# Performance work log

Measured on AMD Instinct MI355X. Metric: run time of the kernel, lower is better.

## Reference

```python
import jax, jax.numpy as jnp
import numpy as np

CH = 512
GROUPS = 8
EPS = 1e-5


def setup_inputs() -> dict:
    key = jax.random.key(0)
    ks = jax.random.split(key, 5)
    B, C, H, W = 16, CH, 32, 32
    x = jax.random.normal(ks[0], (B, C, H, W), dtype=jnp.float32)
    # GroupNorm affine params
    norm_w = jnp.ones((C,), dtype=jnp.float32)
    norm_b = jnp.zeros((C,), dtype=jnp.float32)
    # 1x1 conv == linear over channels; store weights as [out, in]
    qkv_w = jax.random.normal(ks[1], (3 * C, C), dtype=jnp.float32) * (C ** -0.5)
    qkv_b = jnp.zeros((3 * C,), dtype=jnp.float32)
    proj_w = jax.random.normal(ks[2], (C, C), dtype=jnp.float32) * (C ** -0.5)
    proj_b = jnp.zeros((C,), dtype=jnp.float32)
    return {"x": x, "norm_w": norm_w, "norm_b": norm_b,
            "qkv_w": qkv_w, "qkv_b": qkv_b,
            "proj_w": proj_w, "proj_b": proj_b}


def _group_norm(x, w, b):
    B, C, H, W = x.shape
    g = GROUPS
    xg = x.reshape(B, g, C // g, H * W)
    mean = xg.mean(axis=(2, 3), keepdims=True)
    var = xg.var(axis=(2, 3), keepdims=True)
    xn = (xg - mean) * jax.lax.rsqrt(var + EPS)
    xn = xn.reshape(B, C, H, W)
    return xn * w[None, :, None, None] + b[None, :, None, None]


def reference(x, norm_w, norm_b, qkv_w, qkv_b, proj_w, proj_b):
    B, C, H, W = x.shape
    h = _group_norm(x, norm_w, norm_b)  # [B,C,H,W]
    hs = h.reshape(B, C, H * W)  # spatial tokens along last axis
    # 1x1 conv QKV: [3C,C] @ [B,C,N] -> [B,3C,N]
    qkv = jnp.einsum('oc,bcn->bon', qkv_w, hs) + qkv_b[None, :, None]
    q, k, v = jnp.split(qkv, 3, axis=1)  # each [B,C,N]
    scale = C ** (-0.5)
    attn = jnp.einsum('bci,bcj->bij', q, k) * scale  # [B,N,N]
    attn = jax.nn.softmax(attn, axis=-1)
    out = jnp.einsum('bij,bcj->bci', attn, v)  # [B,C,N]
    out = jnp.einsum('oc,bcn->bon', proj_w, out) + proj_b[None, :, None]
    return x + out.reshape(B, C, H, W)
```

## Files before the change

kernel.cpp:

```cpp
#include <hip/hip_runtime.h>
#include <math.h>

#define Bn   16
#define Cn   512
#define Nn   1024
#define Gn   8
#define CPG  64
#define EPSf 1e-5f

typedef short           bf16x8 __attribute__((ext_vector_type(8)));
typedef float           f32x4  __attribute__((ext_vector_type(4)));
typedef unsigned short  u16;
typedef unsigned short  u16x4  __attribute__((ext_vector_type(4)));
typedef unsigned short  u16x8  __attribute__((ext_vector_type(8)));

#define TS 136

__device__ __forceinline__ u16 f2b(float f) {
  union { float f; unsigned u; } c; c.f = f;
  unsigned r = (c.u + 0x7FFFu + ((c.u >> 16) & 1u)) >> 16;
  return (u16)r;
}

__device__ __forceinline__ void g2l16(const void* g, void* l) {
  __builtin_amdgcn_global_load_lds(
      (const __attribute__((address_space(1))) unsigned int*)g,
      (__attribute__((address_space(3))) unsigned int*)l, 16, 0, 0);
}

__device__ __forceinline__ void gemm_core(u16* As, u16* Bs,
    const u16* __restrict__ A, size_t sA,
    const u16* __restrict__ B, size_t sB, int K, f32x4 acc[4][4]) {
  const int t = threadIdx.x;
  const int w = t >> 6, l = t & 63, quad = l >> 4, lr = l & 15;
  const int wm = (w >> 1) * 64, wn = (w & 1) * 64;

  const int ra = w * 16 + (l >> 2);
  const int p  = l & 3;
  const int q  = p ^ ((ra >> 1) & 3);
  const u16* gA0 = A + (size_t)ra * sA + q * 8;
  const u16* gA1 = A + (size_t)(ra + 64) * sA + q * 8;
  const u16* gB0 = B + (size_t)ra * sB + q * 8;
  const u16* gB1 = B + (size_t)(ra + 64) * sB + q * 8;
  u16* lA0 = As + ra * 32 + p * 8;
  u16* lA1 = As + (ra + 64) * 32 + p * 8;
  u16* lB0 = Bs + ra * 32 + p * 8;
  u16* lB1 = Bs + (ra + 64) * 32 + p * 8;

  for (int k0 = 0; k0 < K; k0 += 32) {
    __syncthreads();
    g2l16(gA0 + k0, lA0);
    g2l16(gA1 + k0, lA1);
    g2l16(gB0 + k0, lB0);
    g2l16(gB1 + k0, lB1);
    __syncthreads();
    bf16x8 af[4], bfr[4];
    #pragma unroll
    for (int fm = 0; fm < 4; fm++) {
      int r = wm + fm * 16 + lr;
      af[fm] = *(const bf16x8*)&As[r * 32 + ((quad ^ ((r >> 1) & 3)) << 3)];
    }
    #pragma unroll
    for (int fn = 0; fn < 4; fn++) {
      int r = wn + fn * 16 + lr;
      bfr[fn] = *(const bf16x8*)&Bs[r * 32 + ((quad ^ ((r >> 1) & 3)) << 3)];
    }
    #pragma unroll
    for (int fm = 0; fm < 4; fm++)
      #pragma unroll
      for (int fn = 0; fn < 4; fn++)
        acc[fm][fn] = __builtin_amdgcn_mfma_f32_16x16x32_bf16(
            af[fm], bfr[fn], acc[fm][fn], 0, 0, 0);
  }
}

#define GEMM_PRE()                                              \
  const int t = threadIdx.x;                                    \
  const int w = t >> 6, l = t & 63, quad = l >> 4, lr = l & 15; \
  const int wm = (w >> 1) * 64, wn = (w & 1) * 64;              \
  (void)w; (void)wm; (void)wn; (void)l;                         \
  f32x4 acc[4][4];                                              \
  { f32x4 z = {0.f, 0.f, 0.f, 0.f};                             \
    for (int i_ = 0; i_ < 4; i_++)                              \
      for (int j_ = 0; j_ < 4; j_++) acc[i_][j_] = z; }

#define TILE_FLUSH(T, DST, rowstride)                           \
  {                                                             \
    _Pragma("unroll")                                           \
    for (int k_ = 0; k_ < 4; k_++) {                            \
      int idx = threadIdx.x + 256 * k_;                         \
      int row = idx >> 4, ch = idx & 15;                        \
      u16x8 v_ = *(u16x8*)&T[row * TS + ch * 8];                \
      *(u16x8*)&(DST)[(size_t)row * (rowstride) + ch * 8] = v_; \
    }                                                           \
  }

__global__ __launch_bounds__(256) void prep_k(const float* __restrict__ qkv_w,
    const float* __restrict__ proj_w, const float* __restrict__ qkv_b,
    const float* __restrict__ x, u16* __restrict__ wqk16,
    u16* __restrict__ wvT16, u16* __restrict__ pw16,
    float* __restrict__ bias2, float* __restrict__ stats) {
  __shared__ u16 T[64][68];
  __shared__ float redf[8];
  int bid = blockIdx.x, t = threadIdx.x;
  if (bid < 512) {
    int i = bid * 256 + t;
    float4 v = ((const float4*)qkv_w)[i];
    u16x4 o;
    o.x = f2b(v.x); o.y = f2b(v.y); o.z = f2b(v.z); o.w = f2b(v.w);
    ((u16x4*)wqk16)[i] = o;
  } else if (bid < 576) {
    int tile = bid - 512, tx = tile & 7, ty = tile >> 3;
    int row = t >> 4, col4 = t & 15;
    #pragma unroll
    for (int it = 0; it < 4; it++) {
      int cc = row + it * 16;
      float4 v = *(const float4*)&qkv_w[(size_t)(1024 + ty * 64 + cc) * 512 + tx * 64 + col4 * 4];
      u16x4 o;
      o.x = f2b(v.x); o.y = f2b(v.y); o.z = f2b(v.z); o.w = f2b(v.w);
      *(u16x4*)&T[cc][col4 * 4] = o;
    }
    __syncthreads();
    #pragma unroll
    for (int it = 0; it < 2; it++) {
      int ch = t + it * 256;
      int d = ch >> 3, c8 = (ch & 7) * 8;
      u16x8 o;
      #pragma unroll
      for (int j = 0; j < 8; j++) o[j] = T[c8 + j][d];
      *(u16x8*)&wvT16[(size_t)(tx * 64 + d) * 512 + ty * 64 + c8] = o;
    }
  } else if (bid < 578) {
    int m = (bid - 576) * 256 + t;
    float s = 0.f;
    for (int c = 0; c < 512; c++)
      s += proj_w[(size_t)m * 512 + c] * qkv_b[1024 + c];
    bias2[m] = s;
  } else if (bid < 1090) {
    int idx = bid - 578, bg = idx >> 2, part = idx & 3;
    const float4* xp = (const float4*)x + (size_t)bg * 16384 + part * 4096;
    float s = 0.f, ss = 0.f;
    for (int i = t; i < 4096; i += 256) {
      float4 v = xp[i];
      s  += v.x + v.y + v.z + v.w;
      ss += v.x * v.x + v.y * v.y + v.z * v.z + v.w * v.w;
    }
    #pragma unroll
    for (int off = 32; off > 0; off >>= 1) {
      s  += __shfl_down(s, off);
      ss += __shfl_down(ss, off);
    }
    int lane = t & 63, wid = t >> 6;
    if (lane == 0) { redf[wid] = s; redf[4 + wid] = ss; }
    __syncthreads();
    if (t == 0) {
      atomicAdd(&stats[bg],       redf[0] + redf[1] + redf[2] + redf[3]);
      atomicAdd(&stats[128 + bg], redf[4] + redf[5] + redf[6] + redf[7]);
    }
  } else {
    int i = (bid - 1090) * 256 + t;
    float4 v = ((const float4*)proj_w)[i];
    u16x4 o;
    o.x = f2b(v.x); o.y = f2b(v.y); o.z = f2b(v.z); o.w = f2b(v.w);
    ((u16x4*)pw16)[i] = o;
  }
}

__global__ __launch_bounds__(256) void gnw2_k(const float* __restrict__ x,
    const float* __restrict__ stats, const float* __restrict__ nw,
    const float* __restrict__ nb, const u16* __restrict__ pw16,
    const u16* __restrict__ wvT16, u16* __restrict__ W2, u16* __restrict__ hT) {
  __shared__ u16 AsBs[8192];
  int bid = blockIdx.x;
  if (bid < 16) {
    int m0 = (bid >> 2) * 128, d0 = (bid & 3) * 128;
    GEMM_PRE();
    gemm_core(AsBs, AsBs + 4096, pw16 + (size_t)m0 * 512, 512,
              wvT16 + (size_t)d0 * 512, 512, 512, acc);
    #pragma unroll
    for (int fm = 0; fm < 4; fm++) {
      int m = m0 + wm + fm * 16 + quad * 4;
      #pragma unroll
      for (int fn = 0; fn < 4; fn++) {
        int d = d0 + wn + fn * 16 + lr;
        f32x4 a = acc[fm][fn];
        W2[(size_t)(m    ) * 512 + d] = f2b(a[0]);
        W2[(size_t)(m + 1) * 512 + d] = f2b(a[1]);
        W2[(size_t)(m + 2) * 512 + d] = f2b(a[2]);
        W2[(size_t)(m + 3) * 512 + d] = f2b(a[3]);
      }
    }
    return;
  }
  int u = bid - 16;
  int b = u >> 7, rem = u & 127, c0 = (rem >> 4) * 64, n0 = (rem & 15) * 64;
  u16 (*T)[68] = (u16(*)[68])AsBs;
  int t = threadIdx.x;
  int row = t >> 4, col4 = t & 15;
  const float inv = 1.0f / 65536.0f;
  #pragma unroll
  for (int it = 0; it < 4; it++) {
    int cc = row + it * 16;
    int c  = c0 + cc;
    int bg = b * Gn + (c >> 6);
    float mean = stats[bg] * inv;
    float var  = stats[128 + bg] * inv - mean * mean;
    float rstd = rsqrtf(var + EPSf);
    float a  = nw[c] * rstd;
    float bb = nb[c] - mean * a;
    float4 xv = *(const float4*)&x[((size_t)(b * Cn + c)) * Nn + n0 + col4 * 4];
    u16x4 o;
    o.x = f2b(xv.x * a + bb); o.y = f2b(xv.y * a + bb);
    o.z = f2b(xv.z * a + bb); o.w = f2b(xv.w * a + bb);
    *(u16x4*)&T[cc][col4 * 4] = o;
  }
  __syncthreads();
  #pragma unroll
  for (int it = 0; it < 2; it++) {
    int ch = t + it * 256;
    int n  = ch >> 3, c8 = (ch & 7) * 8;
    u16x8 o;
    #pragma unroll
    for (int j = 0; j < 8; j++) o[j] = T[c8 + j][n];
    *(u16x8*)&hT[((size_t)(b * Nn + n0 + n)) * 512 + c0 + c8] = o;
  }
}

__global__ __launch_bounds__(256) void qkvp_k(const u16* __restrict__ wqk16,
    const u16* __restrict__ W2, const u16* __restrict__ hT,
    const float* __restrict__ qkv_b, u16* __restrict__ qkT,
    u16* __restrict__ VP) {
  __shared__ u16 SH[64 * TS];
  int u = blockIdx.x;
  GEMM_PRE();
  if (u < 1024) {
    int b = u >> 6, rem = u & 63, m0 = (rem >> 3) * 128, n0 = (rem & 7) * 128;
    gemm_core(SH, SH + 4096, wqk16 + (size_t)m0 * 512, 512,
              hT + ((size_t)(b * Nn + n0)) * 512, 512, 512, acc);
    float bss[4][4];
    #pragma unroll
    for (int fm = 0; fm < 4; fm++) {
      int mb = m0 + wm + fm * 16 + quad * 4;
      #pragma unroll
      for (int r = 0; r < 4; r++) bss[fm][r] = qkv_b[mb + r];
    }
    #pragma unroll
    for (int h = 0; h < 2; h++) {
      __syncthreads();
      if ((w & 1) == h) {
        #pragma unroll
        for (int fm = 0; fm < 4; fm++) {
          int mb = wm + fm * 16 + quad * 4;
          #pragma unroll
          for (int fn = 0; fn < 4; fn++) {
            int nl = fn * 16 + lr;
            f32x4 a = acc[fm][fn];
            u16x4 pk;
            pk.x = f2b(a[0] + bss[fm][0]); pk.y = f2b(a[1] + bss[fm][1]);
            pk.z = f2b(a[2] + bss[fm][2]); pk.w = f2b(a[3] + bss[fm][3]);
            *(u16x4*)&SH[nl * TS + mb] = pk;
          }
        }
      }
      __syncthreads();
      u16* dst = qkT + ((size_t)(b * Nn + n0 + h * 64)) * 1024 + m0;
      TILE_FLUSH(SH, dst, 1024);
    }
  } else {
    int u2 = u - 1024;
    int b = u2 >> 5, rem = u2 & 31, m0 = (rem >> 3) * 128, j0 = (rem & 7) * 128;
    gemm_core(SH, SH + 4096, W2 + (size_t)m0 * 512, 512,
              hT + ((size_t)(b * Nn + j0)) * 512, 512, 512, acc);
    #pragma unroll
    for (int h = 0; h < 2; h++) {
      __syncthreads();
      if ((w >> 1) == h) {
        #pragma unroll
        for (int fm = 0; fm < 4; fm++) {
          int ml = fm * 16 + quad * 4;
          #pragma unroll
          for (int fn = 0; fn < 4; fn++) {
            int jl = wn + fn * 16 + lr;
            f32x4 a = acc[fm][fn];
            SH[(ml    ) * TS + jl] = f2b(a[0]);
            SH[(ml + 1) * TS + jl] = f2b(a[1]);
            SH[(ml + 2) * TS + jl] = f2b(a[2]);
            SH[(ml + 3) * TS + jl] = f2b(a[3]);
          }
        }
      }
      __syncthreads();
      u16* dst = VP + ((size_t)(b * 512 + m0 + h * 64)) * 1024 + j0;
      TILE_FLUSH(SH, dst, 1024);
    }
  }
}

__global__ __launch_bounds__(256) void qkexp_k(const u16* __restrict__ qkT,
    u16* __restrict__ Pm, float* __restrict__ rpart) {
  __shared__ u16 SH[64 * TS];
  __shared__ float psum[128];
  int u = blockIdx.x;
  int b = u >> 6, rem = u & 63, i0 = (rem >> 3) * 128, j0 = (rem & 7) * 128;
  const u16* base = qkT + (size_t)b * Nn * 1024;
  GEMM_PRE();
  gemm_core(SH, SH + 4096, base + (size_t)i0 * 1024, 1024,
            base + (size_t)j0 * 1024 + 512, 1024, 512, acc);
  if (t < 128) psum[t] = 0.f;
  __syncthreads();
  const float scale = 0.04419417382415922f;
  #pragma unroll
  for (int fm = 0; fm < 4; fm++) {
    int ri = wm + fm * 16 + quad * 4;
    float rs0 = 0.f, rs1 = 0.f, rs2 = 0.f, rs3 = 0.f;
    #pragma unroll
    for (int fn = 0; fn < 4; fn++) {
      f32x4 a = acc[fm][fn];
      rs0 += __expf(a[0] * scale);
      rs1 += __expf(a[1] * scale);
      rs2 += __expf(a[2] * scale);
      rs3 += __expf(a[3] * scale);
    }
    #pragma unroll
    for (int mask = 1; mask < 16; mask <<= 1) {
      rs0 += __shfl_xor(rs0, mask);
      rs1 += __shfl_xor(rs1, mask);
      rs2 += __shfl_xor(rs2, mask);
      rs3 += __shfl_xor(rs3, mask);
    }
    if (lr == 0) {
      atomicAdd(&psum[ri],     rs0);
      atomicAdd(&psum[ri + 1], rs1);
      atomicAdd(&psum[ri + 2], rs2);
      atomicAdd(&psum[ri + 3], rs3);
    }
  }
  __syncthreads();
  if (t < 128)
    rpart[((size_t)(b * 8) + (rem & 7)) * 1024 + i0 + t] = psum[t];
  #pragma unroll
  for (int h = 0; h < 2; h++) {
    __syncthreads();
    if ((w >> 1) == h) {
      #pragma unroll
      for (int fm = 0; fm < 4; fm++) {
        int il = fm * 16 + quad * 4;
        #pragma unroll
        for (int fn = 0; fn < 4; fn++) {
          int jl = wn + fn * 16 + lr;
          f32x4 a = acc[fm][fn];
          SH[(il    ) * TS + jl] = f2b(__expf(a[0] * scale));
          SH[(il + 1) * TS + jl] = f2b(__expf(a[1] * scale));
          SH[(il + 2) * TS + jl] = f2b(__expf(a[2] * scale));
          SH[(il + 3) * TS + jl] = f2b(__expf(a[3] * scale));
        }
      }
    }
    __syncthreads();
    u16* dst = Pm + ((size_t)(b * Nn + i0 + h * 64)) * 1024 + j0;
    TILE_FLUSH(SH, dst, 1024);
  }
}

__global__ __launch_bounds__(256) void pvout_k(const u16* __restrict__ VP,
    const u16* __restrict__ Pm, const float* __restrict__ rpart,
    const float* __restrict__ bias2, const float* __restrict__ proj_b,
    const float* __restrict__ x, float* __restrict__ out) {
  __shared__ u16 AsBs[8192];
  __shared__ float rinv[128];
  int bid = blockIdx.x;
  int b = bid >> 5, rem = bid & 31, m0 = (rem >> 3) * 128, i0 = (rem & 7) * 128;
  if (threadIdx.x < 128) {
    float s = 0.f;
    #pragma unroll
    for (int jb = 0; jb < 8; jb++)
      s += rpart[((size_t)(b * 8 + jb)) * 1024 + i0 + threadIdx.x];
    rinv[threadIdx.x] = 1.0f / s;
  }
  GEMM_PRE();
  gemm_core(AsBs, AsBs + 4096, VP + ((size_t)(b * 512 + m0)) * 1024, 1024,
            Pm + ((size_t)(b * Nn + i0)) * 1024, 1024, 1024, acc);
  #pragma unroll
  for (int fm = 0; fm < 4; fm++) {
    int m = m0 + wm + fm * 16 + quad * 4;
    float c0 = bias2[m    ] + proj_b[m    ];
    float c1 = bias2[m + 1] + proj_b[m + 1];
    float c2 = bias2[m + 2] + proj_b[m + 2];
    float c3 = bias2[m + 3] + proj_b[m + 3];
    #pragma unroll
    for (int fn = 0; fn < 4; fn++) {
      int il = wn + fn * 16 + lr;
      int i  = i0 + il;
      float ri = rinv[il];
      f32x4 a = acc[fm][fn];
      size_t o0 = ((size_t)(b * Cn + m)) * Nn + i;
      out[o0                  ] = a[0] * ri + c0 + x[o0                  ];
      out[o0 + Nn             ] = a[1] * ri + c1 + x[o0 + Nn             ];
      out[o0 + 2 * Nn         ] = a[2] * ri + c2 + x[o0 + 2 * Nn         ];
      out[o0 + 3 * (size_t)Nn] = a[3] * ri + c3 + x[o0 + 3 * (size_t)Nn];
    }
  }
}

extern "C" void kernel_launch(void* const* d_in, const int* in_sizes, int n_in,
                              void* d_out, int out_size, void* d_ws, size_t ws_size,
                              hipStream_t stream) {
  const float* x      = (const float*)d_in[0];
  const float* norm_w = (const float*)d_in[1];
  const float* norm_b = (const float*)d_in[2];
  const float* qkv_w  = (const float*)d_in[3];
  const float* qkv_b  = (const float*)d_in[4];
  const float* proj_w = (const float*)d_in[5];
  const float* proj_b = (const float*)d_in[6];
  float* out = (float*)d_out;
  char* ws = (char*)d_ws;

  u16*   wqk16 = (u16*)(ws);
  u16*   wvT16 = (u16*)(ws + 1048576);
  u16*   pw16  = (u16*)(ws + 1572864);
  u16*   W2    = (u16*)(ws + 2097152);
  float* bias2 = (float*)(ws + 2621440);
  float* stats = (float*)(ws + 2623488);
  u16*   hT    = (u16*)(ws + 2624512);
  u16*   qkT   = (u16*)(ws + 19401728);
  u16*   VP    = (u16*)(ws + 52956160);
  u16*   Pm    = (u16*)(ws + 69733376);
  float* rpart = (float*)(ws + 103287808);

  hipMemsetAsync(stats, 0, 1024, stream);
  prep_k<<<1346, 256, 0, stream>>>(qkv_w, proj_w, qkv_b, x, wqk16, wvT16,
                                   pw16, bias2, stats);
  gnw2_k<<<2064, 256, 0, stream>>>(x, stats, norm_w, norm_b, pw16, wvT16,
                                   W2, hT);
  qkvp_k<<<1536, 256, 0, stream>>>(wqk16, W2, hT, qkv_b, qkT, VP);
  qkexp_k<<<1024, 256, 0, stream>>>(qkT, Pm, rpart);
  pvout_k<<<512, 256, 0, stream>>>(VP, Pm, rpart, bias2, proj_b, x, out);
}
```

Before: 232.8 us.

## Use 256x128 tiles with triple-buffered async LDS loads in QKV GEMM

Replaces the 128x128 GEMM core in the QKV/VP projection kernel with a 256x128-tile core. Each wave now computes 128x64 outputs, and K-slices are loaded into a three-slot LDS ring through global_load_lds, with one slice prefetched ahead and a single barrier per step. This halves the grid, raises operand reuse per LDS load, and reduces barriers. In exchange it uses more accumulator registers and LDS per block, which can limit occupancy, and it launches fewer blocks. A no-op index change in qkexp_k is also included.

```diff
diff --git a/kernel.cpp b/kernel.cpp
--- a/kernel.cpp
+++ b/kernel.cpp
@@ -26,6 +26,10 @@
   __builtin_amdgcn_global_load_lds(
       (const __attribute__((address_space(1))) unsigned int*)g,
       (__attribute__((address_space(3))) unsigned int*)l, 16, 0, 0);
+}
+
+__device__ __forceinline__ void barrier_asm() {
+  asm volatile("s_barrier" ::: "memory");
 }
 
 __device__ __forceinline__ void gemm_core(u16* As, u16* Bs,
@@ -94,6 +98,71 @@
       *(u16x8*)&(DST)[(size_t)row * (rowstride) + ch * 8] = v_; \
     }                                                           \
   }
+
+#define SLOT 12288
+
+__device__ __forceinline__ void core256(const u16* __restrict__ A, size_t sA,
+    const u16* __restrict__ B, size_t sB, int K, u16* SH, f32x4 acc[8][4],
+    int wm, int wn, int quad, int lr) {
+  const int t = threadIdx.x, wv = t >> 6, l = t & 63;
+  const int srow = l >> 2;
+  const int sch  = ((l & 3) ^ ((l >> 3) & 3)) * 8;
+
+  const u16* gA[4]; int lA[4];
+  const u16* gB[2]; int lB[2];
+  #pragma unroll
+  for (int c = 0; c < 4; c++) {
+    gA[c] = A + (size_t)(wv * 64 + c * 16 + srow) * sA + sch;
+    lA[c] = wv * 2048 + c * 512 + l * 8;
+  }
+  #pragma unroll
+  for (int c = 0; c < 2; c++) {
+    gB[c] = B + (size_t)(wv * 32 + c * 16 + srow) * sB + sch;
+    lB[c] = 8192 + wv * 1024 + c * 512 + l * 8;
+  }
+
+  u16 *sc = SH, *sn = SH + SLOT, *sf = SH + 2 * SLOT;
+  #pragma unroll
+  for (int c = 0; c < 4; c++) g2l16(gA[c], sc + lA[c]);
+  #pragma unroll
+  for (int c = 0; c < 2; c++) g2l16(gB[c], sc + lB[c]);
+
+  const int rch = (quad ^ ((lr >> 1) & 3)) * 8;
+  int aoff[8], boff[4];
+  #pragma unroll
+  for (int fm = 0; fm < 8; fm++) aoff[fm] = (wm + fm * 16 + lr) * 32 + rch;
+  #pragma unroll
+  for (int fn = 0; fn < 4; fn++) boff[fn] = 8192 + (wn + fn * 16 + lr) * 32 + rch;
+
+  const int nt = K >> 5;
+  for (int tt = 0; tt < nt; tt++) {
+    if (tt + 1 < nt) {
+      const int k0 = (tt + 1) * 32;
+      #pragma unroll
+      for (int c = 0; c < 4; c++) g2l16(gA[c] + k0, sn + lA[c]);
+      #pragma unroll
+      for (int c = 0; c < 2; c++) g2l16(gB[c] + k0, sn + lB[c]);
+      asm volatile("s_waitcnt vmcnt(6)" ::: "memory");
+    } else {
+      asm volatile("s_waitcnt vmcnt(0)" ::: "memory");
+    }
+    barrier_asm();
+    bf16x8 af[8], bfr[4];
+    #pragma unroll
+    for (int fm = 0; fm < 8; fm++) af[fm] = *(const bf16x8*)&sc[aoff[fm]];
+    #pragma unroll
+    for (int fn = 0; fn < 4; fn++) bfr[fn] = *(const bf16x8*)&sc[boff[fn]];
+    __builtin_amdgcn_s_setprio(1);
+    #pragma unroll
+    for (int fm = 0; fm < 8; fm++)
+      #pragma unroll
+      for (int fn = 0; fn < 4; fn++)
+        acc[fm][fn] = __builtin_amdgcn_mfma_f32_16x16x32_bf16(
+            af[fm], bfr[fn], acc[fm][fn], 0, 0, 0);
+    __builtin_amdgcn_s_setprio(0);
+    u16* tmp = sc; sc = sn; sn = sf; sf = tmp;
+  }
+}
 
 __global__ __launch_bounds__(256) void prep_k(const float* __restrict__ qkv_w,
     const float* __restrict__ proj_w, const float* __restrict__ qkv_b,
@@ -226,72 +295,90 @@
   }
 }
 
-__global__ __launch_bounds__(256) void qkvp_k(const u16* __restrict__ wqk16,
+__global__ __launch_bounds__(256, 2) void qkvp_k(const u16* __restrict__ wqk16,
     const u16* __restrict__ W2, const u16* __restrict__ hT,
     const float* __restrict__ qkv_b, u16* __restrict__ qkT,
     u16* __restrict__ VP) {
-  __shared__ u16 SH[64 * TS];
+  __shared__ __align__(16) u16 SH[3 * SLOT];
   int u = blockIdx.x;
-  GEMM_PRE();
-  if (u < 1024) {
-    int b = u >> 6, rem = u & 63, m0 = (rem >> 3) * 128, n0 = (rem & 7) * 128;
-    gemm_core(SH, SH + 4096, wqk16 + (size_t)m0 * 512, 512,
-              hT + ((size_t)(b * Nn + n0)) * 512, 512, 512, acc);
-    float bss[4][4];
-    #pragma unroll
-    for (int fm = 0; fm < 4; fm++) {
-      int mb = m0 + wm + fm * 16 + quad * 4;
-      #pragma unroll
-      for (int r = 0; r < 4; r++) bss[fm][r] = qkv_b[mb + r];
-    }
+  const int t = threadIdx.x;
+  const int w = t >> 6, l = t & 63, quad = l >> 4, lr = l & 15;
+  const int wm = (w >> 1) * 128, wn = (w & 1) * 64;
+  f32x4 acc[8][4];
+  { f32x4 z = {0.f, 0.f, 0.f, 0.f};
+    #pragma unroll
+    for (int i_ = 0; i_ < 8; i_++)
+      #pragma unroll
+      for (int j_ = 0; j_ < 4; j_++) acc[i_][j_] = z; }
+
+  if (u < 512) {
+    int b = u >> 5, rem = u & 31, m0 = (rem >> 3) * 256, n0 = (rem & 7) * 128;
+    core256(wqk16 + (size_t)m0 * 512, 512,
+            hT + (size_t)(b * Nn + n0) * 512, 512, 512, SH, acc, wm, wn, quad, lr);
+    float4 bss[8];
+    #pragma unroll
+    for (int fm = 0; fm < 8; fm++)
+      bss[fm] = *(const float4*)&qkv_b[m0 + wm + fm * 16 + quad * 4];
+    u16* T = SH;
+    const int hsel = wn >> 6;
     #pragma unroll
     for (int h = 0; h < 2; h++) {
-      __syncthreads();
-      if ((w & 1) == h) {
+      barrier_asm();
+      if (hsel == h) {
         #pragma unroll
-        for (int fm = 0; fm < 4; fm++) {
-          int mb = wm + fm * 16 + quad * 4;
+        for (int fm = 0; fm < 8; fm++) {
+          int mc = wm + fm * 16 + quad * 4;
           #pragma unroll
           for (int fn = 0; fn < 4; fn++) {
             int nl = fn * 16 + lr;
             f32x4 a = acc[fm][fn];
             u16x4 pk;
-            pk.x = f2b(a[0] + bss[fm][0]); pk.y = f2b(a[1] + bss[fm][1]);
-            pk.z = f2b(a[2] + bss[fm][2]); pk.w = f2b(a[3] + bss[fm][3]);
-            *(u16x4*)&SH[nl * TS + mb] = pk;
+            pk.x = f2b(a[0] + bss[fm].x); pk.y = f2b(a[1] + bss[fm].y);
+            pk.z = f2b(a[2] + bss[fm].z); pk.w = f2b(a[3] + bss[fm].w);
+            *(u16x4*)&T[nl * 264 + mc] = pk;
           }
         }
       }
-      __syncthreads();
-      u16* dst = qkT + ((size_t)(b * Nn + n0 + h * 64)) * 1024 + m0;
-      TILE_FLUSH(SH, dst, 1024);
+      barrier_asm();
+      #pragma unroll
+      for (int kk = 0; kk < 8; kk++) {
+        int idx = t + 256 * kk, row = idx >> 5, grp = idx & 31;
+        u16x8 v = *(u16x8*)&T[row * 264 + grp * 8];
+        *(u16x8*)&qkT[((size_t)(b * Nn + n0 + h * 64 + row)) * 1024 + m0 + grp * 8] = v;
+      }
     }
   } else {
-    int u2 = u - 1024;
-    int b = u2 >> 5, rem = u2 & 31, m0 = (rem >> 3) * 128, j0 = (rem & 7) * 128;
-    gemm_core(SH, SH + 4096, W2 + (size_t)m0 * 512, 512,
-              hT + ((size_t)(b * Nn + j0)) * 512, 512, 512, acc);
+    int u2 = u - 512;
+    int b = u2 >> 4, rem = u2 & 15, m0 = (rem >> 3) * 256, j0 = (rem & 7) * 128;
+    core256(W2 + (size_t)m0 * 512, 512,
+            hT + (size_t)(b * Nn + j0) * 512, 512, 512, SH, acc, wm, wn, quad, lr);
+    u16* T = SH;
+    const int hsel = wm >> 7;
     #pragma unroll
     for (int h = 0; h < 2; h++) {
-      __syncthreads();
-      if ((w >> 1) == h) {
+      barrier_asm();
+      if (hsel == h) {
         #pragma unroll
-        for (int fm = 0; fm < 4; fm++) {
+        for (int fm = 0; fm < 8; fm++) {
           int ml = fm * 16 + quad * 4;
           #pragma unroll
           for (int fn = 0; fn < 4; fn++) {
             int jl = wn + fn * 16 + lr;
             f32x4 a = acc[fm][fn];
-            SH[(ml    ) * TS + jl] = f2b(a[0]);
-            SH[(ml + 1) * TS + jl] = f2b(a[1]);
-            SH[(ml + 2) * TS + jl] = f2b(a[2]);
-            SH[(ml + 3) * TS + jl] = f2b(a[3]);
+            T[(ml    ) * TS + jl] = f2b(a[0]);
+            T[(ml + 1) * TS + jl] = f2b(a[1]);
+            T[(ml + 2) * TS + jl] = f2b(a[2]);
+            T[(ml + 3) * TS + jl] = f2b(a[3]);
           }
         }
       }
-      __syncthreads();
-      u16* dst = VP + ((size_t)(b * 512 + m0 + h * 64)) * 1024 + j0;
-      TILE_FLUSH(SH, dst, 1024);
+      barrier_asm();
+      #pragma unroll
+      for (int kk = 0; kk < 8; kk++) {
+        int idx = t + 256 * kk, row = idx >> 4, grp = idx & 15;
+        u16x8 v = *(u16x8*)&T[row * TS + grp * 8];
+        *(u16x8*)&VP[((size_t)(b * 512 + m0 + h * 128 + row)) * 1024 + j0 + grp * 8] = v;
+      }
     }
   }
 }
@@ -315,7 +402,7 @@
     float rs0 = 0.f, rs1 = 0.f, rs2 = 0.f, rs3 = 0.f;
     #pragma unroll
     for (int fn = 0; fn < 4; fn++) {
-      f32x4 a = acc[fm][fn];
+      f32x4 a = acc[fn >= 0 ? fm : fm][fn];
       rs0 += __expf(a[0] * scale);
       rs1 += __expf(a[1] * scale);
       rs2 += __expf(a[2] * scale);
@@ -432,7 +519,7 @@
                                    pw16, bias2, stats);
   gnw2_k<<<2064, 256, 0, stream>>>(x, stats, norm_w, norm_b, pw16, wvT16,
                                    W2, hT);
-  qkvp_k<<<1536, 256, 0, stream>>>(wqk16, W2, hT, qkv_b, qkT, VP);
+  qkvp_k<<<768, 256, 0, stream>>>(wqk16, W2, hT, qkv_b, qkT, VP);
   qkexp_k<<<1024, 256, 0, stream>>>(qkT, Pm, rpart);
   pvout_k<<<512, 256, 0, stream>>>(VP, Pm, rpart, bias2, proj_b, x, out);
 }
```

Measured after the change: 225.8 us. 3.0% less time.
